# Kernel tuning notes

Measured on AMD Instinct MI355X. Metric: run time of the kernel, lower is better.

The kernel has to match this reference:

```python
import jax, jax.numpy as jnp
import numpy as np

B, N, C = 8, 2048, 320
CQ = C // 5  # query/key channel dim = 64


def setup_inputs() -> dict:
    key = jax.random.key(0)
    ks = jax.random.split(key, 8)
    s = 0.05
    return {
        "x": jax.random.normal(ks[0], (B, N, C), dtype=jnp.float32),
        "Wq": jax.random.normal(ks[1], (CQ, C), dtype=jnp.float32) * s,
        "bq": jax.random.normal(ks[2], (CQ,), dtype=jnp.float32) * s,
        "Wk": jax.random.normal(ks[3], (CQ, C), dtype=jnp.float32) * s,
        "bk": jax.random.normal(ks[4], (CQ,), dtype=jnp.float32) * s,
        "Wv": jax.random.normal(ks[5], (C, C), dtype=jnp.float32) * s,
        "bv": jax.random.normal(ks[6], (C,), dtype=jnp.float32) * s,
        "gamma": jnp.zeros((1,), dtype=jnp.float32) + 0.5,
    }


def reference(x, Wq, bq, Wk, bk, Wv, bv, gamma):
    # x: (B, N, C). torch module permutes to (B, C, N) and uses 1x1 Conv1d,
    # which is a per-position linear over channels.
    q = jnp.einsum("bnc,qc->bnq", x, Wq) + bq          # (B, N, CQ) proj_query
    k = jnp.einsum("bnc,qc->bqn", x, Wk) + bk[:, None]  # (B, CQ, N) proj_key
    energy = jnp.einsum("bnq,bqm->bnm", q, k)           # (B, N, N)
    attention = jax.nn.softmax(energy, axis=-1)          # softmax over last dim
    v = jnp.einsum("bnc,dc->bdn", x, Wv) + bv[:, None]  # (B, C, N) proj_value
    # torch: out = bmm(V (B,C,N), A (B,N,N)) -> out[b,c,n] = sum_k V[b,c,k]*A[b,k,n]
    out = jnp.einsum("bck,bkn->bcn", v, attention)       # (B, C, N)
    out = gamma[0] * out + jnp.swapaxes(x, 1, 2)         # residual on (B, C, N)
    return jnp.swapaxes(out, 1, 2)                       # (B, N, C)
```

## Files before the change

### kernel.cpp

```cpp
#include <hip/hip_runtime.h>
#include <hip/hip_bf16.h>

#define BB 8
#define NN 2048
#define CC 320
#define CQ 64
#define LOG2E 1.4426950408889634f

typedef __attribute__((ext_vector_type(8)))  short bf16x8;
typedef __attribute__((ext_vector_type(4)))  float f32x4;
typedef __attribute__((ext_vector_type(16))) float f32x16;
typedef __attribute__((ext_vector_type(4)))  unsigned short us4;
typedef __attribute__((ext_vector_type(8)))  unsigned short us8;
typedef __attribute__((ext_vector_type(4)))  unsigned int u32x4;
typedef unsigned short u16;


static __device__ __forceinline__ u16 f2b(float f) {
  unsigned u = __builtin_bit_cast(unsigned, f);
  unsigned r = (u + 0x7FFFu + ((u >> 16) & 1u)) >> 16;
  return (u16)r;
}
static __device__ __forceinline__ float b2f(u16 s) {
  unsigned u = ((unsigned)s) << 16;
  return __builtin_bit_cast(float, u);
}

static __device__ __forceinline__ f32x16 zero16() {
  f32x16 v = {0,0,0,0, 0,0,0,0, 0,0,0,0, 0,0,0,0};
  return v;
}
static __device__ __forceinline__ f32x4 zero4() {
  f32x4 v = {0,0,0,0};
  return v;
}

static __device__ __forceinline__ void gll16(const void* g, void* l) {
  __builtin_amdgcn_global_load_lds(
      (const __attribute__((address_space(1))) unsigned int*)g,
      (__attribute__((address_space(3))) unsigned int*)l, 16, 0, 0);
}

static __device__ __forceinline__ bf16x8 cvt8(float4 a, float4 b) {
  unsigned p0, p1, p2, p3;
  asm("v_cvt_pk_bf16_f32 %0, %1, %2" : "=v"(p0) : "v"(a.x), "v"(a.y));
  asm("v_cvt_pk_bf16_f32 %0, %1, %2" : "=v"(p1) : "v"(a.z), "v"(a.w));
  asm("v_cvt_pk_bf16_f32 %0, %1, %2" : "=v"(p2) : "v"(b.x), "v"(b.y));
  asm("v_cvt_pk_bf16_f32 %0, %1, %2" : "=v"(p3) : "v"(b.z), "v"(b.w));
  u32x4 w = {p0, p1, p2, p3};
  return __builtin_bit_cast(bf16x8, w);
}

__global__ __launch_bounds__(256) void cvt_blk(const float* __restrict__ x,
                                               const float* __restrict__ Wq,
                                               const float* __restrict__ Wk,
                                               const float* __restrict__ Wv,
                                               u16* __restrict__ X3,
                                               u16* __restrict__ W3) {
  __shared__ float xs[32][324];
  const int t = threadIdx.x;
  const int bid = blockIdx.x;
  const bool isX = (bid < 512);
  const int b = isX ? bid : (bid - 512);
#pragma unroll
  for (int i = 0; i < 10; ++i) {
    const int lidx = i * 256 + t;
    const int m = lidx / 80;
    const int kq = lidx - m * 80;
    const float* src;
    if (isX) {
      src = x + (size_t)(b * 32 + m) * CC;
    } else {
      const int row = b * 32 + m;
      src = (row < 64) ? (Wq + (size_t)row * CC)
          : (row < 128) ? (Wk + (size_t)(row - 64) * CC)
                        : (Wv + (size_t)(row - 128) * CC);
    }
    float4 v = *(const float4*)(src + kq * 4);
    *(float4*)&xs[m][kq * 4] = v;
  }
  __syncthreads();
  u16* dst0 = (isX ? X3 : W3) + (size_t)b * 10240;
#pragma unroll
  for (int i = 0; i < 5; ++i) {
    const int u = i * 256 + t;
    const int kk8 = u >> 5, ml = u & 31;
    float4 a = *(const float4*)&xs[ml][kk8 * 8];
    float4 c = *(const float4*)&xs[ml][kk8 * 8 + 4];
    bf16x8 o = cvt8(a, c);
    *(bf16x8*)(dst0 + (size_t)u * 8) = o;
  }
}

__global__ __launch_bounds__(256) void gemm_qkv(
    const u16* __restrict__ X3, const u16* __restrict__ W3,
    const float* __restrict__ bq, const float* __restrict__ bk,
    const float* __restrict__ bv,
    u16* __restrict__ Qb, u16* __restrict__ Kb, u16* __restrict__ Vt) {
  const int tid = threadIdx.x;
  const int lane = tid & 63, wid = tid >> 6;
  const int r = lane & 31, h = lane >> 5;
  const int bid = blockIdx.x;
  const int xcd = bid & 7;
  const int slot = bid >> 3;
  const int colt = slot & 3;
  const int yG = slot >> 2;
  const int ytile = yG * 8 + xcd;
  const int m0 = ytile * 128 + wid * 32;
  const int col0 = colt * 128;
  const int NT = (colt == 3) ? 2 : 4;
  const int mt = m0 >> 5;

  const u16* abase = X3 + (size_t)mt * 10240 + (size_t)h * 256 + r * 8;
  const u16* bbase0 = W3 + (size_t)(colt * 4 + 0) * 10240 + (size_t)h * 256 + r * 8;
  const u16* bbase1 = bbase0 + 10240;
  const u16* bbase2 = bbase0 + 20480;
  const u16* bbase3 = bbase0 + 30720;

  f32x16 acc0 = zero16(), acc1 = zero16(), acc2 = zero16(), acc3 = zero16();
  bf16x8 a  = *(const bf16x8*)(abase);
  bf16x8 b0 = *(const bf16x8*)(bbase0);
  bf16x8 b1 = *(const bf16x8*)(bbase1);
  bf16x8 b2, b3;
  if (NT == 4) {
    b2 = *(const bf16x8*)(bbase2);
    b3 = *(const bf16x8*)(bbase3);
  }
#pragma unroll 1
  for (int ks = 0; ks < 20; ++ks) {
    bf16x8 na, nb0, nb1, nb2, nb3;
    if (ks < 19) {
      na  = *(const bf16x8*)(abase  + (ks + 1) * 512);
      nb0 = *(const bf16x8*)(bbase0 + (ks + 1) * 512);
      nb1 = *(const bf16x8*)(bbase1 + (ks + 1) * 512);
      if (NT == 4) {
        nb2 = *(const bf16x8*)(bbase2 + (ks + 1) * 512);
        nb3 = *(const bf16x8*)(bbase3 + (ks + 1) * 512);
      }
    }
    acc0 = __builtin_amdgcn_mfma_f32_32x32x16_bf16(a, b0, acc0, 0, 0, 0);
    acc1 = __builtin_amdgcn_mfma_f32_32x32x16_bf16(a, b1, acc1, 0, 0, 0);
    if (NT == 4) {
      acc2 = __builtin_amdgcn_mfma_f32_32x32x16_bf16(a, b2, acc2, 0, 0, 0);
      acc3 = __builtin_amdgcn_mfma_f32_32x32x16_bf16(a, b3, acc3, 0, 0, 0);
    }
    a = na; b0 = nb0; b1 = nb1;
    if (NT == 4) { b2 = nb2; b3 = nb3; }
  }

  const int bb = m0 >> 11;
  const int mloc = m0 & 2047;

#pragma unroll
  for (int nt = 0; nt < 4; ++nt) {
    if (nt >= NT) continue;
    const int tb = col0 + nt * 32;
    const int col = tb + r;
    const f32x16 A = (nt == 0) ? acc0 : (nt == 1) ? acc1 : (nt == 2) ? acc2 : acc3;
    if (tb >= 128) {
      const int c = col - 128;
      const float bias = bv[c];
      u16* vdst = Vt + (((size_t)(bb * 256 + (mloc >> 3)) * 320 + c) * 8) + 4 * h;
#pragma unroll
      for (int g = 0; g < 4; ++g) {
        us4 o;
#pragma unroll
        for (int e = 0; e < 4; ++e) o[e] = f2b(A[g * 4 + e] + bias);
        *(us4*)(vdst + (size_t)g * 2560) = o;
      }
    } else if (tb >= 64) {
      const float bias = bk[col - 64];
#pragma unroll
      for (int reg = 0; reg < 16; ++reg) {
        const int row = m0 + (reg & 3) + 8 * (reg >> 2) + 4 * h;
        Kb[(size_t)row * CQ + (col - 64)] = f2b(A[reg] + bias);
      }
    } else {
      const float bias = bq[col];
      const int kt = mloc >> 5;
      u16* qdst = Qb + (((size_t)(bb * 64 + kt) * 8 + (col >> 3)) * 32) * 8 + (col & 7);
#pragma unroll
      for (int reg = 0; reg < 16; ++reg) {
        const int kl = (reg & 3) + 8 * (reg >> 2) + 4 * h;
        qdst[kl * 8] = f2b((A[reg] + bias) * LOG2E);
      }
    }
  }
}

__global__ __launch_bounds__(512) void row_stats(
    const u16* __restrict__ Qb, const u16* __restrict__ Kb,
    float* __restrict__ Lb) {
  __shared__ float Sp[8][64];
  const int tid = threadIdx.x;
  const int lane = tid & 63, wid = tid >> 6;
  const int rl = lane & 15, hq = lane >> 4;
  const int bid = blockIdx.x;
  const int batch = bid & 7;
  const int kloc64 = (bid >> 3) * 64;

  bf16x8 af[4][2];
#pragma unroll
  for (int mt = 0; mt < 4; ++mt) {
    const int k_loc = kloc64 + mt * 16 + rl;
    const int kt = k_loc >> 5, kl = k_loc & 31;
#pragma unroll
    for (int qs = 0; qs < 2; ++qs)
      af[mt][qs] = *(const bf16x8*)(Qb +
          (((size_t)(batch * 64 + kt) * 8 + qs * 4 + hq) * 32 + kl) * 8);
  }

  float S[4][4];
#pragma unroll
  for (int mt = 0; mt < 4; ++mt)
#pragma unroll
    for (int rr = 0; rr < 4; ++rr) S[mt][rr] = 0.f;

  const int mstart = batch * NN + wid * 256;
  const u16* kr = Kb + (size_t)(mstart + rl) * CQ + hq * 8;
  bf16x8 c0 = *(const bf16x8*)(kr);
  bf16x8 c1 = *(const bf16x8*)(kr + 32);
#pragma unroll 1
  for (int ms = 0; ms < 16; ++ms) {
    bf16x8 n0, n1;
    if (ms < 15) {
      n0 = *(const bf16x8*)(kr + 16 * CQ);
      n1 = *(const bf16x8*)(kr + 16 * CQ + 32);
    }
#pragma unroll
    for (int mt = 0; mt < 4; ++mt) {
      f32x4 e = zero4();
      e = __builtin_amdgcn_mfma_f32_16x16x32_bf16(af[mt][0], c0, e, 0, 0, 0);
      e = __builtin_amdgcn_mfma_f32_16x16x32_bf16(af[mt][1], c1, e, 0, 0, 0);
#pragma unroll
      for (int rr = 0; rr < 4; ++rr) S[mt][rr] += __builtin_amdgcn_exp2f(e[rr]);
    }
    c0 = n0; c1 = n1; kr += 16 * CQ;
  }

#pragma unroll
  for (int d = 1; d < 16; d <<= 1)
#pragma unroll
    for (int mt = 0; mt < 4; ++mt)
#pragma unroll
      for (int rr = 0; rr < 4; ++rr) S[mt][rr] += __shfl_xor(S[mt][rr], d, 64);

  if (rl == 0) {
#pragma unroll
    for (int mt = 0; mt < 4; ++mt)
#pragma unroll
      for (int rr = 0; rr < 4; ++rr) Sp[wid][mt * 16 + hq * 4 + rr] = S[mt][rr];
  }
  __syncthreads();
  if (tid < 64) {
    float s = 0.f;
#pragma unroll
    for (int p = 0; p < 8; ++p) s += Sp[p][tid];
    Lb[batch * NN + kloc64 + tid] = __log2f(s);
  }
}

__global__ __launch_bounds__(256, 2) void attn(
    const u16* __restrict__ Qb, const u16* __restrict__ Kb,
    const u16* __restrict__ Vt, const float* __restrict__ Lb,
    const float* __restrict__ x, const float* __restrict__ gamma,
    float* __restrict__ out) {
  __shared__ __align__(16) char LDSRAW[49152];
  float* Ls = (float*)(LDSRAW + 40960);
  const int tid = threadIdx.x;
  const int lane = tid & 63, wid = tid >> 6;
  const int wn = wid >> 1;
  const int kh = wid & 1;
  const int r = lane & 31, h = lane >> 5;
  const int bid = blockIdx.x;
  const int b = bid & 7;
  const int rest = bid >> 3;
  const int ch = rest & 1;
  const int n0 = (rest >> 1) * 64;

#pragma unroll
  for (int i = 0; i < 8; ++i)
    Ls[i * 256 + tid] = Lb[b * NN + i * 256 + tid];

  bf16x8 kf[4];
  {
    const u16* krow = Kb + (size_t)(b * NN + n0 + wn * 32 + r) * CQ + h * 8;
#pragma unroll
    for (int qs = 0; qs < 4; ++qs) kf[qs] = *(const bf16x8*)(krow + qs * 16);
  }

  f32x16 acc[5];
#pragma unroll
  for (int j = 0; j < 5; ++j) acc[j] = zero16();

  const u16* qb3 = Qb + ((size_t)(b * 64 + kh * 32) * 8) * 256 + (size_t)r * 8;
  const float* lsb = Ls + kh * 1024 + 4 * h;

#define STAGE(TN, BUF) {                                                       \
    _Pragma("unroll")                                                          \
    for (int i_ = 0; i_ < 5; ++i_) {                                           \
      const int c_ = wid * 5 + i_;                                             \
      const int khc_ = c_ / 10;                                                \
      const int rem_ = c_ % 10;                                                \
      char* dst_ = LDSRAW + (BUF) * 20480 + khc_ * 10240 + rem_ * 1024;        \
      const int off_ = rem_ * 512 + lane * 8;                                  \
      const int row_ = off_ / 1280;                                            \
      const int win_ = off_ - row_ * 1280;                                     \
      const u16* src_ = Vt +                                                   \
          ((size_t)(b * 256 + khc_ * 128 + (TN) * 4 + row_) * 320              \
           + ch * 160) * 8 + win_;                                             \
      gll16(src_, dst_);                                                       \
    }                                                                          \
  }

#define LQ(QN, TN) {                                                           \
    _Pragma("unroll")                                                          \
    for (int qs = 0; qs < 4; ++qs)                                             \
      QN[qs] = *(const bf16x8*)(qb3 + ((size_t)(TN) * 8 + qs * 2 + h) * 256);  \
  }

#define COMPUTE(T, BUF, QF, QN, TNX) {                                         \
    LQ(QN, TNX)                                                                \
    float4 LF0 = *(const float4*)(lsb + (T) * 32);                             \
    float4 LF1 = *(const float4*)(lsb + (T) * 32 + 8);                         \
    float4 LF2 = *(const float4*)(lsb + (T) * 32 + 16);                        \
    float4 LF3 = *(const float4*)(lsb + (T) * 32 + 24);                        \
    const char* base_ = LDSRAW + (BUF) * 20480 + kh * 10240;                   \
    f32x16 e = zero16();                                                       \
    _Pragma("unroll")                                                          \
    for (int qs = 0; qs < 4; ++qs)                                             \
      e = __builtin_amdgcn_mfma_f32_32x32x16_bf16(QF[qs], kf[qs], e, 0, 0, 0); \
    bf16x8 vf[5][2];                                                           \
    _Pragma("unroll")                                                          \
    for (int j = 0; j < 5; ++j)                                                \
      _Pragma("unroll")                                                        \
      for (int ks = 0; ks < 2; ++ks)                                           \
        vf[j][ks] = *(const bf16x8*)(base_ + (ks * 2 + h) * 2560               \
                                     + (j * 32 + r) * 16);                     \
    unsigned pk0, pk1, pk2, pk3, pk4, pk5, pk6, pk7;                           \
    { float l0 = __builtin_amdgcn_exp2f(e[0]  - LF0.x);                        \
      float h0 = __builtin_amdgcn_exp2f(e[1]  - LF0.y);                        \
      float l1 = __builtin_amdgcn_exp2f(e[2]  - LF0.z);                        \
      float h1 = __builtin_amdgcn_exp2f(e[3]  - LF0.w);                        \
      float l2 = __builtin_amdgcn_exp2f(e[4]  - LF1.x);                        \
      float h2 = __builtin_amdgcn_exp2f(e[5]  - LF1.y);                        \
      float l3 = __builtin_amdgcn_exp2f(e[6]  - LF1.z);                        \
      float h3 = __builtin_amdgcn_exp2f(e[7]  - LF1.w);                        \
      float l4 = __builtin_amdgcn_exp2f(e[8]  - LF2.x);                        \
      float h4 = __builtin_amdgcn_exp2f(e[9]  - LF2.y);                        \
      float l5 = __builtin_amdgcn_exp2f(e[10] - LF2.z);                        \
      float h5 = __builtin_amdgcn_exp2f(e[11] - LF2.w);                        \
      float l6 = __builtin_amdgcn_exp2f(e[12] - LF3.x);                        \
      float h6 = __builtin_amdgcn_exp2f(e[13] - LF3.y);                        \
      float l7 = __builtin_amdgcn_exp2f(e[14] - LF3.z);                        \
      float h7 = __builtin_amdgcn_exp2f(e[15] - LF3.w);                        \
      asm("v_cvt_pk_bf16_f32 %0, %1, %2" : "=v"(pk0) : "v"(l0), "v"(h0));      \
      asm("v_cvt_pk_bf16_f32 %0, %1, %2" : "=v"(pk1) : "v"(l1), "v"(h1));      \
      asm("v_cvt_pk_bf16_f32 %0, %1, %2" : "=v"(pk2) : "v"(l2), "v"(h2));      \
      asm("v_cvt_pk_bf16_f32 %0, %1, %2" : "=v"(pk3) : "v"(l3), "v"(h3));      \
      asm("v_cvt_pk_bf16_f32 %0, %1, %2" : "=v"(pk4) : "v"(l4), "v"(h4));      \
      asm("v_cvt_pk_bf16_f32 %0, %1, %2" : "=v"(pk5) : "v"(l5), "v"(h5));      \
      asm("v_cvt_pk_bf16_f32 %0, %1, %2" : "=v"(pk6) : "v"(l6), "v"(h6));      \
      asm("v_cvt_pk_bf16_f32 %0, %1, %2" : "=v"(pk7) : "v"(l7), "v"(h7)); }    \
    asm("v_permlane32_swap_b32 %0, %1" : "+v"(pk0), "+v"(pk2));                \
    asm("v_permlane32_swap_b32 %0, %1" : "+v"(pk1), "+v"(pk3));                \
    asm("v_permlane32_swap_b32 %0, %1" : "+v"(pk4), "+v"(pk6));                \
    asm("v_permlane32_swap_b32 %0, %1" : "+v"(pk5), "+v"(pk7));                \
    u32x4 w0_ = {pk0, pk1, pk2, pk3};                                          \
    u32x4 w1_ = {pk4, pk5, pk6, pk7};                                          \
    bf16x8 pa0 = __builtin_bit_cast(bf16x8, w0_);                              \
    bf16x8 pa1 = __builtin_bit_cast(bf16x8, w1_);                              \
    __builtin_amdgcn_s_setprio(1);                                             \
    _Pragma("unroll")                                                          \
    for (int j = 0; j < 5; ++j) {                                              \
      acc[j] = __builtin_amdgcn_mfma_f32_32x32x16_bf16(pa0, vf[j][0], acc[j], 0, 0, 0); \
      acc[j] = __builtin_amdgcn_mfma_f32_32x32x16_bf16(pa1, vf[j][1], acc[j], 0, 0, 0); \
    }                                                                          \
    __builtin_amdgcn_s_setprio(0);                                             \
  }

  bf16x8 qfA[4], qfB[4];

  STAGE(0, 0);
  LQ(qfA, 0)
  __syncthreads();
#pragma unroll 1
  for (int t = 0; t < 32; t += 2) {
    STAGE(t + 1, 1);
    COMPUTE(t, 0, qfA, qfB, t + 1);
    __syncthreads();
    if (t + 2 < 32) STAGE(t + 2, 0);
    COMPUTE(t + 1, 1, qfB, qfA, (t + 2) & 31);
    __syncthreads();
  }
#undef STAGE
#undef LQ
#undef COMPUTE

  float* red = (float*)LDSRAW;
  if (kh == 1) {
#pragma unroll
    for (int reg = 0; reg < 16; ++reg) {
      const int nl = (reg & 3) + 8 * (reg >> 2) + 4 * h;
#pragma unroll
      for (int j = 0; j < 5; ++j)
        red[wn * 5120 + nl * 160 + j * 32 + r] = acc[j][reg];
    }
  }
  __syncthreads();
  if (kh == 0) {
    const float g = gamma[0];
#pragma unroll
    for (int reg = 0; reg < 16; ++reg) {
      const int nl = (reg & 3) + 8 * (reg >> 2) + 4 * h;
      const size_t rowb = ((size_t)(b * NN) + n0 + wn * 32 + nl) * CC + ch * 160 + r;
#pragma unroll
      for (int j = 0; j < 5; ++j) {
        const size_t idx = rowb + (size_t)(j * 32);
        const float s = acc[j][reg] + red[wn * 5120 + nl * 160 + j * 32 + r];
        out[idx] = g * s + x[idx];
      }
    }
  }
}

extern "C" void kernel_launch(void* const* d_in, const int* in_sizes, int n_in,
                              void* d_out, int out_size, void* d_ws, size_t ws_size,
                              hipStream_t stream) {
  const float* x     = (const float*)d_in[0];
  const float* Wq    = (const float*)d_in[1];
  const float* bq    = (const float*)d_in[2];
  const float* Wk    = (const float*)d_in[3];
  const float* bk    = (const float*)d_in[4];
  const float* Wv    = (const float*)d_in[5];
  const float* bv    = (const float*)d_in[6];
  const float* gamma = (const float*)d_in[7];
  float* out = (float*)d_out;

  char* w = (char*)d_ws;
  u16* X3   = (u16*)(w);
  u16* W3   = (u16*)(w + 10485760);
  u16* Qb   = (u16*)(w + 10772480);
  u16* Kb   = (u16*)(w + 12869632);
  u16* Vt   = (u16*)(w + 14966784);
  float* Lb = (float*)(w + 25452544);

  cvt_blk<<<526, 256, 0, stream>>>(x, Wq, Wk, Wv, X3, W3);
  gemm_qkv<<<512, 256, 0, stream>>>(X3, W3, bq, bk, bv, Qb, Kb, Vt);
  row_stats<<<256, 512, 0, stream>>>(Qb, Kb, Lb);
  attn<<<512, 256, 0, stream>>>(Qb, Kb, Vt, Lb, x, gamma, out);
}
```

Measured before the change: 77.74 us.

## Double stage depth to 64-key tiles and read row stats from global

Each pipeline stage in the attention kernel now loads 64 keys of V into LDS instead of 32 and processes them as two 32-key sub-steps. That halves the number of barriers and stage iterations, and LDS grows to 80 KB of dynamic shared memory. The log-sum statistics are no longer copied into LDS; they are read straight from global memory each step. The larger LDS footprint may limit blocks per CU, and the direct global reads add latency in the inner loop.

```diff
diff --git a/kernel.cpp b/kernel.cpp
--- a/kernel.cpp
+++ b/kernel.cpp
@@ -265,8 +265,7 @@
     const u16* __restrict__ Vt, const float* __restrict__ Lb,
     const float* __restrict__ x, const float* __restrict__ gamma,
     float* __restrict__ out) {
-  __shared__ __align__(16) char LDSRAW[49152];
-  float* Ls = (float*)(LDSRAW + 40960);
+  extern __shared__ __align__(16) char LDSRAW[];
   const int tid = threadIdx.x;
   const int lane = tid & 63, wid = tid >> 6;
   const int wn = wid >> 1;
@@ -278,10 +277,6 @@
   const int ch = rest & 1;
   const int n0 = (rest >> 1) * 64;
 
-#pragma unroll
-  for (int i = 0; i < 8; ++i)
-    Ls[i * 256 + tid] = Lb[b * NN + i * 256 + tid];
-
   bf16x8 kf[4];
   {
     const u16* krow = Kb + (size_t)(b * NN + n0 + wn * 32 + r) * CQ + h * 8;
@@ -294,38 +289,37 @@
   for (int j = 0; j < 5; ++j) acc[j] = zero16();
 
   const u16* qb3 = Qb + ((size_t)(b * 64 + kh * 32) * 8) * 256 + (size_t)r * 8;
-  const float* lsb = Ls + kh * 1024 + 4 * h;
-
-#define STAGE(TN, BUF) {                                                       \
+  const float* lbase = Lb + b * NN + kh * 1024 + 4 * h;
+
+#define STAGE64(TN, BUF) {                                                     \
     _Pragma("unroll")                                                          \
-    for (int i_ = 0; i_ < 5; ++i_) {                                           \
-      const int c_ = wid * 5 + i_;                                             \
-      const int khc_ = c_ / 10;                                                \
-      const int rem_ = c_ % 10;                                                \
-      char* dst_ = LDSRAW + (BUF) * 20480 + khc_ * 10240 + rem_ * 1024;        \
+    for (int i_ = 0; i_ < 10; ++i_) {                                          \
+      const int c_ = wid * 10 + i_;                                            \
+      const int khc_ = c_ / 20;                                                \
+      const int rem_ = c_ % 20;                                                \
+      char* dst_ = LDSRAW + (BUF) * 40960 + khc_ * 20480 + rem_ * 1024;        \
       const int off_ = rem_ * 512 + lane * 8;                                  \
       const int row_ = off_ / 1280;                                            \
       const int win_ = off_ - row_ * 1280;                                     \
       const u16* src_ = Vt +                                                   \
-          ((size_t)(b * 256 + khc_ * 128 + (TN) * 4 + row_) * 320              \
+          ((size_t)(b * 256 + khc_ * 128 + (TN) * 8 + row_) * 320              \
            + ch * 160) * 8 + win_;                                             \
       gll16(src_, dst_);                                                       \
     }                                                                          \
   }
 
-#define LQ(QN, TN) {                                                           \
+#define LQ(QN, KT32) {                                                         \
     _Pragma("unroll")                                                          \
     for (int qs = 0; qs < 4; ++qs)                                             \
-      QN[qs] = *(const bf16x8*)(qb3 + ((size_t)(TN) * 8 + qs * 2 + h) * 256);  \
-  }
-
-#define COMPUTE(T, BUF, QF, QN, TNX) {                                         \
-    LQ(QN, TNX)                                                                \
-    float4 LF0 = *(const float4*)(lsb + (T) * 32);                             \
-    float4 LF1 = *(const float4*)(lsb + (T) * 32 + 8);                         \
-    float4 LF2 = *(const float4*)(lsb + (T) * 32 + 16);                        \
-    float4 LF3 = *(const float4*)(lsb + (T) * 32 + 24);                        \
-    const char* base_ = LDSRAW + (BUF) * 20480 + kh * 10240;                   \
+      QN[qs] = *(const bf16x8*)(qb3 + ((size_t)(KT32) * 8 + qs * 2 + h) * 256);\
+  }
+
+#define COMPUTE32(KT32, BUF, SOFF, QF) {                                       \
+    float4 LF0 = *(const float4*)(lbase + (KT32) * 32);                        \
+    float4 LF1 = *(const float4*)(lbase + (KT32) * 32 + 8);                    \
+    float4 LF2 = *(const float4*)(lbase + (KT32) * 32 + 16);                   \
+    float4 LF3 = *(const float4*)(lbase + (KT32) * 32 + 24);                   \
+    const char* base_ = LDSRAW + (BUF) * 40960 + kh * 20480 + (SOFF);          \
     f32x16 e = zero16();                                                       \
     _Pragma("unroll")                                                          \
     for (int qs = 0; qs < 4; ++qs)                                             \
@@ -379,23 +373,29 @@
     __builtin_amdgcn_s_setprio(0);                                             \
   }
 
-  bf16x8 qfA[4], qfB[4];
-
-  STAGE(0, 0);
+  bf16x8 qfA[4], qfB[4], qfs1[4];
+
+  STAGE64(0, 0);
   LQ(qfA, 0)
   __syncthreads();
 #pragma unroll 1
-  for (int t = 0; t < 32; t += 2) {
-    STAGE(t + 1, 1);
-    COMPUTE(t, 0, qfA, qfB, t + 1);
+  for (int t = 0; t < 16; t += 2) {
+    STAGE64(t + 1, 1);
+    LQ(qfB, (t + 1) * 2)
+    LQ(qfs1, t * 2 + 1)
+    COMPUTE32(t * 2,     0, 0,     qfA);
+    COMPUTE32(t * 2 + 1, 0, 10240, qfs1);
     __syncthreads();
-    if (t + 2 < 32) STAGE(t + 2, 0);
-    COMPUTE(t + 1, 1, qfB, qfA, (t + 2) & 31);
+    if (t + 2 < 16) STAGE64(t + 2, 0);
+    LQ(qfA, ((t + 2) & 15) * 2)
+    LQ(qfs1, (t + 1) * 2 + 1)
+    COMPUTE32((t + 1) * 2,     1, 0,     qfB);
+    COMPUTE32((t + 1) * 2 + 1, 1, 10240, qfs1);
     __syncthreads();
   }
-#undef STAGE
+#undef STAGE64
 #undef LQ
-#undef COMPUTE
+#undef COMPUTE32
 
   float* red = (float*)LDSRAW;
   if (kh == 1) {
@@ -448,5 +448,5 @@
   cvt_blk<<<526, 256, 0, stream>>>(x, Wq, Wk, Wv, X3, W3);
   gemm_qkv<<<512, 256, 0, stream>>>(X3, W3, bq, bk, bv, Qb, Kb, Vt);
   row_stats<<<256, 512, 0, stream>>>(Qb, Kb, Lb);
-  attn<<<512, 256, 0, stream>>>(Qb, Kb, Vt, Lb, x, gamma, out);
-}
+  attn<<<512, 256, 81920, stream>>>(Qb, Kb, Vt, Lb, x, gamma, out);
+}
```

Measured after the change: 98.06 us. 26.1% more time.
